# Kernel tuning notes

Measured on AMD Instinct MI355X. Metric: run time of the kernel, lower is better.

Reference implementation:

```python
import jax, jax.numpy as jnp
import numpy as np

N_NODES = 100_000
N_EDGES = 1_600_000
N_GRAPHS = 512
NF = 64        # n_node_feats
H1 = 128       # hidden width
H2 = 64        # dim_node_emb
DIM_OUT = 1
STEPS = 4      # set2set processing steps


def _lin(x, W, b):
    # torch Linear convention: y = x @ W.T + b, W: [out, in]
    return x @ W.T + b


def _gelu(x):
    return jax.nn.gelu(x, approximate=False)  # torch.nn.GELU default (erf)


def _lstm_cell(x, h, c, Wih, Whh, bih, bhh):
    g = x @ Wih.T + bih + h @ Whh.T + bhh
    i, f, gg, o = jnp.split(g, 4, axis=-1)  # torch gate order: i, f, g, o
    i, f, o = jax.nn.sigmoid(i), jax.nn.sigmoid(f), jax.nn.sigmoid(o)
    gg = jnp.tanh(gg)
    c = f * c + i * gg
    h = o * jnp.tanh(c)
    return h, c


def setup_inputs() -> dict:
    key = jax.random.key(0)
    ks = jax.random.split(key, 24)
    p = lambda k, shp: jax.random.normal(k, shp, dtype=jnp.float32) * 0.05
    inp = {
        "x": jax.random.normal(ks[0], (N_NODES, NF), dtype=jnp.float32),
        "edge_index": jax.random.randint(ks[1], (2, N_EDGES), 0, N_NODES, dtype=jnp.int32),
        "batch": jnp.sort(jax.random.randint(ks[2], (N_NODES,), 0, N_GRAPHS, dtype=jnp.int32)),
        "nfc_W": p(ks[3], (H1, NF)), "nfc_b": p(ks[4], (H1,)),
        "gc1_W": p(ks[5], (H1, H1)), "gc1_b": p(ks[6], (H1,)),
        "gc2_W": p(ks[7], (H2, H1)), "gc2_b": p(ks[8], (H2,)),
        "lstm0_Wih": p(ks[9], (4 * H2, 2 * H2)), "lstm0_Whh": p(ks[10], (4 * H2, H2)),
        "lstm0_bih": p(ks[11], (4 * H2,)), "lstm0_bhh": p(ks[12], (4 * H2,)),
        "lstm1_Wih": p(ks[13], (4 * H2, H2)), "lstm1_Whh": p(ks[14], (4 * H2, H2)),
        "lstm1_bih": p(ks[15], (4 * H2,)), "lstm1_bhh": p(ks[16], (4 * H2,)),
        "fc1_W": p(ks[17], (32, 2 * H2)), "fc1_b": p(ks[18], (32,)),
        "fc2_W": p(ks[19], (DIM_OUT, 32)), "fc2_b": p(ks[20], (DIM_OUT,)),
    }
    return inp


def _forward(x, edge_index, batch, nfc_W, nfc_b, gc1_W, gc1_b, gc2_W, gc2_b,
             lstm0_Wih, lstm0_Whh, lstm0_bih, lstm0_bhh,
             lstm1_Wih, lstm1_Whh, lstm1_bih, lstm1_bhh,
             fc1_W, fc1_b, fc2_W, fc2_b):
    src, dst = edge_index[0], edge_index[1]

    def gin_conv(h, W, b):
        # PyG GINConv, eps=0: lin((1+eps)*x + sum_{j in N(i)} x_j)
        agg = jax.ops.segment_sum(h[src], dst, num_segments=N_NODES)
        return _lin(h + agg, W, b)

    h = _gelu(_lin(x, nfc_W, nfc_b))
    h = _gelu(gin_conv(h, gc1_W, gc1_b))
    h = _gelu(gin_conv(h, gc2_W, gc2_b))
    # F.normalize(p=2, dim=1)
    h = h / jnp.maximum(jnp.linalg.norm(h, axis=1, keepdims=True), 1e-12)

    # Set2Set: 2-layer LSTM, 4 processing steps, scatter-softmax attention
    B = N_GRAPHS
    h0 = jnp.zeros((B, H2), jnp.float32); c0 = jnp.zeros((B, H2), jnp.float32)
    h1 = jnp.zeros((B, H2), jnp.float32); c1 = jnp.zeros((B, H2), jnp.float32)
    q_star = jnp.zeros((B, 2 * H2), jnp.float32)
    for _ in range(STEPS):
        h0, c0 = _lstm_cell(q_star, h0, c0, lstm0_Wih, lstm0_Whh, lstm0_bih, lstm0_bhh)
        h1, c1 = _lstm_cell(h0, h1, c1, lstm1_Wih, lstm1_Whh, lstm1_bih, lstm1_bhh)
        q = h1  # [B, H2]
        e = jnp.sum(h * q[batch], axis=-1, keepdims=True)  # [N, 1]
        m = jax.ops.segment_max(e, batch, num_segments=B)
        ex = jnp.exp(e - m[batch])
        s = jax.ops.segment_sum(ex, batch, num_segments=B)
        a = ex / (s[batch] + 1e-16)
        r = jax.ops.segment_sum(a * h, batch, num_segments=B)  # [B, H2]
        q_star = jnp.concatenate([q, r], axis=-1)

    z = _gelu(_lin(q_star, fc1_W, fc1_b))
    z = _lin(z, fc2_W, fc2_b)
    return z, h


def reference(x, edge_index, batch, nfc_W, nfc_b, gc1_W, gc1_b, gc2_W, gc2_b,
              lstm0_Wih, lstm0_Whh, lstm0_bih, lstm0_bhh,
              lstm1_Wih, lstm1_Whh, lstm1_bih, lstm1_bhh,
              fc1_W, fc1_b, fc2_W, fc2_b):
    return _forward(x, edge_index, batch, nfc_W, nfc_b, gc1_W, gc1_b, gc2_W, gc2_b,
                    lstm0_Wih, lstm0_Whh, lstm0_bih, lstm0_bhh,
                    lstm1_Wih, lstm1_Whh, lstm1_bih, lstm1_bhh,
                    fc1_W, fc1_b, fc2_W, fc2_b)
```

## Files before the change

kernel.cpp:

```cpp
#include <hip/hip_runtime.h>
#include <hip/hip_bf16.h>
#include <hip/hip_fp16.h>
#include <math.h>

constexpr int N  = 100000;
constexpr int E  = 1600000;
constexpr int NG = 512;
constexpr int NF = 64;
constexpr int H1 = 128;
constexpr int H2 = 64;

constexpr int BW   = 128;
constexpr int NB   = (N + BW - 1) / BW;
constexpr int CAP  = 2600;
constexpr int CHUNK = 4096;

constexpr int MAXN = 416;
constexpr int RST  = 68;

typedef __attribute__((ext_vector_type(8))) short short8;
typedef __attribute__((ext_vector_type(4))) float f32x4;

__device__ __forceinline__ float gelu_f(float x) {
    return 0.5f * x * (1.0f + erff(x * 0.70710678118654752f));
}
__device__ __forceinline__ float sigmoid_f(float x) {
    return 1.0f / (1.0f + expf(-x));
}
__device__ __forceinline__ float waveAllSum(float v) {
    #pragma unroll
    for (int m = 32; m; m >>= 1) v += __shfl_xor(v, m);
    return v;
}
__device__ __forceinline__ unsigned short f2bf(float x) {
    __hip_bfloat16 b = __float2bfloat16(x);
    return *reinterpret_cast<unsigned short*>(&b);
}
__device__ __forceinline__ float bf2f(unsigned short u) {
    return __uint_as_float(((unsigned int)u) << 16);
}
__device__ __forceinline__ float bf_lo(unsigned int u) { return __uint_as_float(u << 16); }
__device__ __forceinline__ float bf_hi(unsigned int u) { return __uint_as_float(u & 0xffff0000u); }

__device__ __forceinline__ void bfsplit(float v, unsigned short& hi, unsigned short& lo) {
    hi = f2bf(v);
    lo = f2bf(v - bf2f(hi));
}

__global__ __launch_bounds__(256) void setup_kernel(const int* __restrict__ batch,
                                                    const float* __restrict__ Wih0, const float* __restrict__ Whh0,
                                                    const float* __restrict__ bih0, const float* __restrict__ bhh0,
                                                    const float* __restrict__ Wih1, const float* __restrict__ Whh1,
                                                    const float* __restrict__ bih1, const float* __restrict__ bhh1,
                                                    const float* __restrict__ gc1W, const float* __restrict__ gc2W,
                                                    float* __restrict__ WT0, float* __restrict__ WT1,
                                                    float* __restrict__ b0, float* __restrict__ b1,
                                                    unsigned short* __restrict__ W1F, unsigned short* __restrict__ W2F,
                                                    int* __restrict__ bcursor, int* __restrict__ gstart) {
    int i = blockIdx.x * 256 + threadIdx.x;
    if (i < 192 * 256) {
        int k = i >> 8, j = i & 255;
        WT0[i] = (k < 128) ? Wih0[j * 128 + k] : Whh0[j * 64 + (k - 128)];
    }
    if (i < 128 * 256) {
        int k = i >> 8, j = i & 255;
        WT1[i] = (k < 64) ? Wih1[j * 64 + k] : Whh1[j * 64 + (k - 64)];
    }
    if (i < 16384) {
        int f = i >> 9, r = i & 511, l = r >> 3, j = r & 7;
        int c = f >> 3, ct = f & 7;
        int o = ct * 16 + (l & 15), k = c * 32 + (l >> 4) * 8 + j;
        unsigned short hi, lo;
        bfsplit(gc1W[o * 128 + k], hi, lo);
        W1F[f * 1024 + r] = hi;
        W1F[f * 1024 + 512 + r] = lo;
    }
    if (i < 8192) {
        int f = i >> 9, r = i & 511, l = r >> 3, j = r & 7;
        int c2 = f >> 2, ct2 = f & 3;
        int o = ct2 * 16 + (l & 15), k = c2 * 32 + (l >> 4) * 8 + j;
        unsigned short hi, lo;
        bfsplit(gc2W[o * 128 + k], hi, lo);
        W2F[f * 1024 + r] = hi;
        W2F[f * 1024 + 512 + r] = lo;
    }
    if (i < 256) { b0[i] = bih0[i] + bhh0[i]; b1[i] = bih1[i] + bhh1[i]; }
    if (i < NB) bcursor[i] = i * CAP;
    if (i <= NG) {
        if (i == NG) gstart[NG] = N;
        else {
            int lo = 0, hi = N;
            while (lo < hi) {
                int mid = (lo + hi) >> 1;
                if (batch[mid] < i) lo = mid + 1; else hi = mid;
            }
            gstart[i] = lo;
        }
    }
}

__global__ __launch_bounds__(256) void bin_scatter_kernel(const int* __restrict__ ei,
                                                          int* __restrict__ bcursor,
                                                          int* __restrict__ pairs) {
    __shared__ int hist[NB];
    __shared__ int start_s[NB];
    __shared__ int lcur[NB];
    int tid = threadIdx.x;
    int e0 = blockIdx.x * CHUNK;
    for (int b = tid; b < NB; b += 256) hist[b] = 0;
    __syncthreads();
    #pragma unroll 4
    for (int k = 0; k < CHUNK / 256; ++k) {
        int e = e0 + k * 256 + tid;
        if (e < E) atomicAdd(&hist[ei[E + e] >> 7], 1);
    }
    __syncthreads();
    for (int b = tid; b < NB; b += 256) {
        if (hist[b]) start_s[b] = atomicAdd(&bcursor[b], hist[b]);
        lcur[b] = 0;
    }
    __syncthreads();
    #pragma unroll 4
    for (int k = 0; k < CHUNK / 256; ++k) {
        int e = e0 + k * 256 + tid;
        if (e < E) {
            int d = ei[E + e];
            int s = ei[e];
            int b = d >> 7;
            int pos = start_s[b] + atomicAdd(&lcur[b], 1);
            if (pos < (b + 1) * CAP) pairs[pos] = (s << 7) | (d & 127);
        }
    }
}

__global__ __launch_bounds__(256) void csr_bucket_kernel(const int* __restrict__ pairs,
                                                         const int* __restrict__ bcursor,
                                                         int* __restrict__ srcs,
                                                         int2* __restrict__ nrange) {
    __shared__ int cnt_l[BW];
    __shared__ int cur_l[BW];
    __shared__ int wt[2];
    int b = blockIdx.x;
    int tid = threadIdx.x;
    int base = b * CAP;
    int cnt = bcursor[b] - base;
    if (cnt > CAP) cnt = CAP;
    if (tid < BW) cnt_l[tid] = 0;
    __syncthreads();
    for (int i = tid; i < cnt; i += 256) {
        atomicAdd(&cnt_l[pairs[base + i] & 127], 1);
    }
    __syncthreads();
    if (tid < BW) {
        int v = cnt_l[tid];
        int lane = tid & 63, w = tid >> 6;
        int incl = v;
        #pragma unroll
        for (int off = 1; off < 64; off <<= 1) {
            int t = __shfl_up(incl, off);
            if (lane >= off) incl += t;
        }
        if (lane == 63) wt[w] = incl;
        __syncthreads();
        int excl = (w ? wt[0] : 0) + incl - v;
        int node = b * BW + tid;
        if (node < N) nrange[node] = make_int2(base + excl, base + excl + v);
        cur_l[tid] = excl;
    } else {
        __syncthreads();
    }
    __syncthreads();
    for (int i = tid; i < cnt; i += 256) {
        int p = pairs[base + i];
        int pos = atomicAdd(&cur_l[p & 127], 1);
        srcs[base + pos] = p >> 7;
    }
}

template <int ID, int OD>
__global__ __launch_bounds__(256) void lin_mfma_kernel(const float* __restrict__ in,
                                                       const float* __restrict__ W,
                                                       const float* __restrict__ bias,
                                                       unsigned short* __restrict__ out_bf, int nrows) {
    constexpr int KC = 32;
    constexpr int NCH = ID / KC;
    constexpr int AST = 40;
    constexpr int NCT = OD / 16;
    constexpr int LDSU = 2 * 128 * AST + 2 * OD * AST;
    __shared__ __align__(16) unsigned short lds[LDSU];
    unsigned short* Ahi = lds;
    unsigned short* Alo = lds + 128 * AST;
    unsigned short* Whi = lds + 2 * 128 * AST;
    unsigned short* Wlo = lds + 2 * 128 * AST + OD * AST;

    int tid = threadIdx.x;
    int w = tid >> 6, lane = tid & 63;
    int m15 = lane & 15, quad = lane >> 4;
    int nb = blockIdx.x * 128;

    f32x4 acc[2][NCT];
    #pragma unroll
    for (int rt = 0; rt < 2; ++rt)
        #pragma unroll
        for (int ct = 0; ct < NCT; ++ct) acc[rt][ct] = (f32x4)0.f;

    for (int c = 0; c < NCH; ++c) {
        int kb = c * KC;
        #pragma unroll
        for (int it = 0; it < 4; ++it) {
            int f4 = it * 256 + tid;
            int row = f4 >> 3, kq = (f4 & 7) * 4;
            float4 v = make_float4(0.f, 0.f, 0.f, 0.f);
            if (nb + row < nrows) v = *(const float4*)&in[(size_t)(nb + row) * ID + kb + kq];
            unsigned short h0, h1, h2, h3, l0, l1, l2, l3;
            bfsplit(v.x, h0, l0); bfsplit(v.y, h1, l1);
            bfsplit(v.z, h2, l2); bfsplit(v.w, h3, l3);
            uint2 uh, ul;
            uh.x = (unsigned int)h0 | ((unsigned int)h1 << 16);
            uh.y = (unsigned int)h2 | ((unsigned int)h3 << 16);
            ul.x = (unsigned int)l0 | ((unsigned int)l1 << 16);
            ul.y = (unsigned int)l2 | ((unsigned int)l3 << 16);
            *(uint2*)&Ahi[row * AST + kq] = uh;
            *(uint2*)&Alo[row * AST + kq] = ul;
        }
        #pragma unroll
        for (int it = 0; it < OD / 32; ++it) {
            int f4 = it * 256 + tid;
            int o = f4 >> 3, kq = (f4 & 7) * 4;
            float4 v = *(const float4*)&W[(size_t)o * ID + kb + kq];
            unsigned short h0, h1, h2, h3, l0, l1, l2, l3;
            bfsplit(v.x, h0, l0); bfsplit(v.y, h1, l1);
            bfsplit(v.z, h2, l2); bfsplit(v.w, h3, l3);
            uint2 uh, ul;
            uh.x = (unsigned int)h0 | ((unsigned int)h1 << 16);
            uh.y = (unsigned int)h2 | ((unsigned int)h3 << 16);
            ul.x = (unsigned int)l0 | ((unsigned int)l1 << 16);
            ul.y = (unsigned int)l2 | ((unsigned int)l3 << 16);
            *(uint2*)&Whi[o * AST + kq] = uh;
            *(uint2*)&Wlo[o * AST + kq] = ul;
        }
        __syncthreads();

        short8 ah0 = *(const short8*)&Ahi[(w * 32 + m15) * AST + quad * 8];
        short8 ah1 = *(const short8*)&Ahi[(w * 32 + 16 + m15) * AST + quad * 8];
        short8 al0 = *(const short8*)&Alo[(w * 32 + m15) * AST + quad * 8];
        short8 al1 = *(const short8*)&Alo[(w * 32 + 16 + m15) * AST + quad * 8];
        #pragma unroll
        for (int ct = 0; ct < NCT; ++ct) {
            short8 bh = *(const short8*)&Whi[(ct * 16 + m15) * AST + quad * 8];
            short8 bl = *(const short8*)&Wlo[(ct * 16 + m15) * AST + quad * 8];
            acc[0][ct] = __builtin_amdgcn_mfma_f32_16x16x32_bf16(ah0, bh, acc[0][ct], 0, 0, 0);
            acc[0][ct] = __builtin_amdgcn_mfma_f32_16x16x32_bf16(ah0, bl, acc[0][ct], 0, 0, 0);
            acc[0][ct] = __builtin_amdgcn_mfma_f32_16x16x32_bf16(al0, bh, acc[0][ct], 0, 0, 0);
            acc[1][ct] = __builtin_amdgcn_mfma_f32_16x16x32_bf16(ah1, bh, acc[1][ct], 0, 0, 0);
            acc[1][ct] = __builtin_amdgcn_mfma_f32_16x16x32_bf16(ah1, bl, acc[1][ct], 0, 0, 0);
            acc[1][ct] = __builtin_amdgcn_mfma_f32_16x16x32_bf16(al1, bh, acc[1][ct], 0, 0, 0);
        }
        __syncthreads();
    }

    float bcol[NCT];
    #pragma unroll
    for (int ct = 0; ct < NCT; ++ct) bcol[ct] = bias[ct * 16 + m15];

    constexpr int EPS = OD + 8;
    unsigned short* ep = lds;
    #pragma unroll
    for (int rt = 0; rt < 2; ++rt)
        #pragma unroll
        for (int ct = 0; ct < NCT; ++ct)
            #pragma unroll
            for (int r = 0; r < 4; ++r) {
                int rl = w * 32 + rt * 16 + quad * 4 + r;
                float v = gelu_f(acc[rt][ct][r] + bcol[ct]);
                ep[rl * EPS + ct * 16 + m15] = f2bf(v);
            }
    __syncthreads();
    constexpr int U4 = 128 * OD / 8;
    for (int i = tid; i < U4; i += 256) {
        int row = i / (OD / 8);
        int off = (i % (OD / 8)) * 8;
        int grow = nb + row;
        if (grow < nrows) {
            uint4 v = *(const uint4*)&ep[row * EPS + off];
            *(uint4*)(out_bf + (size_t)grow * OD + off) = v;
        }
    }
}

__global__ __launch_bounds__(256) void agg_kernel(const uint2* __restrict__ hb2,
                                                  const int2* __restrict__ nrange,
                                                  const int* __restrict__ srcs,
                                                  uint4* __restrict__ utab) {
    int wave = threadIdx.x >> 6, lane = threadIdx.x & 63;
    int half = lane >> 5, hl = lane & 31;
    int n = blockIdx.x * 4 + wave;
    if (n >= N) return;
    int2 rng = nrange[n];
    int s0 = rng.x, deg = rng.y - rng.x;
    int m1 = deg < 64 ? deg : 64;
    int pre = (lane < m1) ? srcs[s0 + lane] : 0;
    float a0 = 0.f, a1 = 0.f, a2 = 0.f, a3 = 0.f;
    int t = 0;
    for (; t + 8 <= m1; t += 8) {
        int i0 = __shfl(pre, t + half);
        int i1 = __shfl(pre, t + 2 + half);
        int i2 = __shfl(pre, t + 4 + half);
        int i3 = __shfl(pre, t + 6 + half);
        uint2 u0 = hb2[(size_t)i0 * 32 + hl];
        uint2 u1 = hb2[(size_t)i1 * 32 + hl];
        uint2 u2 = hb2[(size_t)i2 * 32 + hl];
        uint2 u3 = hb2[(size_t)i3 * 32 + hl];
        a0 += bf_lo(u0.x); a1 += bf_hi(u0.x); a2 += bf_lo(u0.y); a3 += bf_hi(u0.y);
        a0 += bf_lo(u1.x); a1 += bf_hi(u1.x); a2 += bf_lo(u1.y); a3 += bf_hi(u1.y);
        a0 += bf_lo(u2.x); a1 += bf_hi(u2.x); a2 += bf_lo(u2.y); a3 += bf_hi(u2.y);
        a0 += bf_lo(u3.x); a1 += bf_hi(u3.x); a2 += bf_lo(u3.y); a3 += bf_hi(u3.y);
    }
    for (; t < m1; t += 2) {
        int idx = t + half;
        int idc = idx < m1 ? idx : 0;
        int s = __shfl(pre, idc);
        if (idx < m1) {
            uint2 u = hb2[(size_t)s * 32 + hl];
            a0 += bf_lo(u.x); a1 += bf_hi(u.x); a2 += bf_lo(u.y); a3 += bf_hi(u.y);
        }
    }
    for (int j = 64 + half; j < deg; j += 2) {
        int s = srcs[s0 + j];
        uint2 u = hb2[(size_t)s * 32 + hl];
        a0 += bf_lo(u.x); a1 += bf_hi(u.x); a2 += bf_lo(u.y); a3 += bf_hi(u.y);
    }
    a0 += __shfl_down(a0, 32);
    a1 += __shfl_down(a1, 32);
    a2 += __shfl_down(a2, 32);
    a3 += __shfl_down(a3, 32);
    if (half == 0) {
        uint2 u = hb2[(size_t)n * 32 + hl];
        a0 += bf_lo(u.x); a1 += bf_hi(u.x); a2 += bf_lo(u.y); a3 += bf_hi(u.y);
        unsigned short h0, h1, h2, h3, l0, l1, l2, l3;
        bfsplit(a0, h0, l0); bfsplit(a1, h1, l1);
        bfsplit(a2, h2, l2); bfsplit(a3, h3, l3);
        uint4 o;
        o.x = (unsigned int)h0 | ((unsigned int)h1 << 16);
        o.y = (unsigned int)h2 | ((unsigned int)h3 << 16);
        o.z = (unsigned int)l0 | ((unsigned int)l1 << 16);
        o.w = (unsigned int)l2 | ((unsigned int)l3 << 16);
        utab[(size_t)n * 32 + hl] = o;
    }
}

__global__ __launch_bounds__(256, 3) void lin2_fused_kernel(const uint4* __restrict__ in4,
                                                            const uint4* __restrict__ W1F,
                                                            const float* __restrict__ b1,
                                                            const uint4* __restrict__ W2F,
                                                            unsigned short* __restrict__ y2,
                                                            int nrows) {
    constexpr int AST2 = 40;
    __shared__ __align__(16) unsigned short lds[4 * 2560];
    union U8 { uint4 u; short8 s; };
    int tid = threadIdx.x, w = tid >> 6, lane = tid & 63;
    int m15 = lane & 15, quad = lane >> 4;
    unsigned short* myL = lds + w * 2560;
    int rowbase = blockIdx.x * 128 + w * 32;
    int r0 = rowbase + m15;      if (r0 >= nrows) r0 = nrows - 1;
    int r1 = rowbase + 16 + m15; if (r1 >= nrows) r1 = nrows - 1;
    const uint4* a0p = in4 + (size_t)r0 * 32 + quad * 2;
    const uint4* a1p = in4 + (size_t)r1 * 32 + quad * 2;

    float bc[8];
    #pragma unroll
    for (int ct = 0; ct < 8; ++ct) bc[ct] = b1[ct * 16 + m15];

    f32x4 acc[2][8];
    #pragma unroll
    for (int rt = 0; rt < 2; ++rt)
        #pragma unroll
        for (int ct = 0; ct < 8; ++ct) acc[rt][ct] = (f32x4)0.f;

    #pragma unroll
    for (int c = 0; c < 4; ++c) {
        uint4 u00 = a0p[c * 8], u01 = a0p[c * 8 + 1];
        uint4 u10 = a1p[c * 8], u11 = a1p[c * 8 + 1];
        U8 t;
        t.u = make_uint4(u00.x, u00.y, u01.x, u01.y); short8 ah0 = t.s;
        t.u = make_uint4(u00.z, u00.w, u01.z, u01.w); short8 al0 = t.s;
        t.u = make_uint4(u10.x, u10.y, u11.x, u11.y); short8 ah1 = t.s;
        t.u = make_uint4(u10.z, u10.w, u11.z, u11.w); short8 al1 = t.s;
        #pragma unroll
        for (int ct = 0; ct < 8; ++ct) {
            U8 th, tl;
            th.u = W1F[(c * 8 + ct) * 128 + lane];
            tl.u = W1F[(c * 8 + ct) * 128 + 64 + lane];
            short8 bh = th.s, bl = tl.s;
            acc[0][ct] = __builtin_amdgcn_mfma_f32_16x16x32_bf16(ah0, bh, acc[0][ct], 0, 0, 0);
            acc[0][ct] = __builtin_amdgcn_mfma_f32_16x16x32_bf16(ah0, bl, acc[0][ct], 0, 0, 0);
            acc[0][ct] = __builtin_amdgcn_mfma_f32_16x16x32_bf16(al0, bh, acc[0][ct], 0, 0, 0);
            acc[1][ct] = __builtin_amdgcn_mfma_f32_16x16x32_bf16(ah1, bh, acc[1][ct], 0, 0, 0);
            acc[1][ct] = __builtin_amdgcn_mfma_f32_16x16x32_bf16(ah1, bl, acc[1][ct], 0, 0, 0);
            acc[1][ct] = __builtin_amdgcn_mfma_f32_16x16x32_bf16(al1, bh, acc[1][ct], 0, 0, 0);
        }
    }

    #pragma unroll
    for (int ct = 0; ct < 8; ++ct)
        #pragma unroll
        for (int rt = 0; rt < 2; ++rt)
            #pragma unroll
            for (int r = 0; r < 4; ++r)
                acc[rt][ct][r] = gelu_f(acc[rt][ct][r] + bc[ct]);

    unsigned short* Ahi2 = myL;
    unsigned short* Alo2 = myL + 32 * AST2;
    f32x4 acc2[2][4];
    #pragma unroll
    for (int rt = 0; rt < 2; ++rt)
        #pragma unroll
        for (int ct = 0; ct < 4; ++ct) acc2[rt][ct] = (f32x4)0.f;

    #pragma unroll
    for (int c2 = 0; c2 < 4; ++c2) {
        #pragma unroll
        for (int rt = 0; rt < 2; ++rt)
            #pragma unroll
            for (int cc = 0; cc < 2; ++cc) {
                int ct = c2 * 2 + cc;
                #pragma unroll
                for (int r = 0; r < 4; ++r) {
                    int node = rt * 16 + quad * 4 + r;
                    unsigned short hi, lo;
                    bfsplit(acc[rt][ct][r], hi, lo);
                    Ahi2[node * AST2 + cc * 16 + m15] = hi;
                    Alo2[node * AST2 + cc * 16 + m15] = lo;
                }
            }
        asm volatile("s_waitcnt lgkmcnt(0)" ::: "memory");
        short8 ah0 = *(const short8*)&Ahi2[m15 * AST2 + quad * 8];
        short8 ah1 = *(const short8*)&Ahi2[(16 + m15) * AST2 + quad * 8];
        short8 al0 = *(const short8*)&Alo2[m15 * AST2 + quad * 8];
        short8 al1 = *(const short8*)&Alo2[(16 + m15) * AST2 + quad * 8];
        #pragma unroll
        for (int ct2 = 0; ct2 < 4; ++ct2) {
            U8 th, tl;
            th.u = W2F[(c2 * 4 + ct2) * 128 + lane];
            tl.u = W2F[(c2 * 4 + ct2) * 128 + 64 + lane];
            short8 bh = th.s, bl = tl.s;
            acc2[0][ct2] = __builtin_amdgcn_mfma_f32_16x16x32_bf16(ah0, bh, acc2[0][ct2], 0, 0, 0);
            acc2[0][ct2] = __builtin_amdgcn_mfma_f32_16x16x32_bf16(ah0, bl, acc2[0][ct2], 0, 0, 0);
            acc2[0][ct2] = __builtin_amdgcn_mfma_f32_16x16x32_bf16(al0, bh, acc2[0][ct2], 0, 0, 0);
            acc2[1][ct2] = __builtin_amdgcn_mfma_f32_16x16x32_bf16(ah1, bh, acc2[1][ct2], 0, 0, 0);
            acc2[1][ct2] = __builtin_amdgcn_mfma_f32_16x16x32_bf16(ah1, bl, acc2[1][ct2], 0, 0, 0);
            acc2[1][ct2] = __builtin_amdgcn_mfma_f32_16x16x32_bf16(al1, bh, acc2[1][ct2], 0, 0, 0);
        }
    }

    unsigned short* ep = myL;
    #pragma unroll
    for (int rt = 0; rt < 2; ++rt)
        #pragma unroll
        for (int ct2 = 0; ct2 < 4; ++ct2)
            #pragma unroll
            for (int r = 0; r < 4; ++r) {
                int node = rt * 16 + quad * 4 + r;
                __half hv = __float2half(acc2[rt][ct2][r]);
                ep[node * 72 + ct2 * 16 + m15] = *reinterpret_cast<unsigned short*>(&hv);
            }
    asm volatile("s_waitcnt lgkmcnt(0)" ::: "memory");
    #pragma unroll
    for (int it = 0; it < 4; ++it) {
        int idx = it * 64 + lane;
        int rowl = idx >> 3, off = (idx & 7) * 8;
        int grow = rowbase + rowl;
        if (grow < nrows)
            *(uint4*)(y2 + (size_t)grow * 64 + off) = *(const uint4*)&ep[rowl * 72 + off];
    }
}

__global__ __launch_bounds__(256) void agg2_norm_kernel(const uint2* __restrict__ y2,
                                                        const int2* __restrict__ nrange,
                                                        const int* __restrict__ srcs,
                                                        const float* __restrict__ b2,
                                                        float* __restrict__ hn) {
    int wave = threadIdx.x >> 6, lane = threadIdx.x & 63;
    int qw = lane >> 4, ql = lane & 15;
    int n = blockIdx.x * 4 + wave;
    if (n >= N) return;
    int2 rng = nrange[n];
    int s0 = rng.x, deg = rng.y - rng.x;
    int m1 = deg < 64 ? deg : 64;
    int pre = (lane < m1) ? srcs[s0 + lane] : 0;
    float a0 = 0.f, a1 = 0.f, a2 = 0.f, a3 = 0.f;
    auto addu = [&](uint2 u) {
        float2 f01 = __half22float2(*reinterpret_cast<__half2*>(&u.x));
        float2 f23 = __half22float2(*reinterpret_cast<__half2*>(&u.y));
        a0 += f01.x; a1 += f01.y; a2 += f23.x; a3 += f23.y;
    };
    int t = 0;
    for (; t + 8 <= m1; t += 8) {
        int i0 = __shfl(pre, t + qw);
        int i1 = __shfl(pre, t + 4 + qw);
        uint2 u0 = y2[(size_t)i0 * 16 + ql];
        uint2 u1 = y2[(size_t)i1 * 16 + ql];
        addu(u0); addu(u1);
    }
    for (; t < m1; t += 4) {
        int idx = t + qw;
        int s = __shfl(pre, idx < m1 ? idx : 0);
        if (idx < m1) addu(y2[(size_t)s * 16 + ql]);
    }
    for (int j = 64 + qw; j < deg; j += 4) addu(y2[(size_t)srcs[s0 + j] * 16 + ql]);
    a0 += __shfl_down(a0, 32); a1 += __shfl_down(a1, 32);
    a2 += __shfl_down(a2, 32); a3 += __shfl_down(a3, 32);
    a0 += __shfl_down(a0, 16); a1 += __shfl_down(a1, 16);
    a2 += __shfl_down(a2, 16); a3 += __shfl_down(a3, 16);
    if (qw == 0) {
        addu(y2[(size_t)n * 16 + ql]);
        float4 bv = *(const float4*)&b2[ql * 4];
        float v0 = gelu_f(a0 + bv.x), v1 = gelu_f(a1 + bv.y);
        float v2 = gelu_f(a2 + bv.z), v3 = gelu_f(a3 + bv.w);
        float ss = v0 * v0 + v1 * v1 + v2 * v2 + v3 * v3;
        #pragma unroll
        for (int mm = 1; mm < 16; mm <<= 1) ss += __shfl_xor(ss, mm);
        float d = fmaxf(sqrtf(ss), 1e-12f);
        *(float4*)&hn[(size_t)n * 64 + ql * 4] = make_float4(v0 / d, v1 / d, v2 / d, v3 / d);
    }
}

__global__ __launch_bounds__(256) void set2set_kernel(const float* __restrict__ hn,
                                                      const int* __restrict__ gstart,
                                                      const float* __restrict__ WT0, const float* __restrict__ b0,
                                                      const float* __restrict__ WT1, const float* __restrict__ b1,
                                                      float* __restrict__ qstar_out) {
    __shared__ __align__(16) unsigned short hL[MAXN * RST];
    __shared__ float av[MAXN];
    __shared__ __align__(16) float xc0[192];
    __shared__ __align__(16) float xc1[128];
    __shared__ __align__(16) float gates[256];
    __shared__ float c0v[H2], c1v[H2];
    __shared__ float red[4];
    __shared__ float rp[4][H2];
    __shared__ float sp[4];

    int g = blockIdx.x;
    int tid = threadIdx.x, w = tid >> 6, lane = tid & 63;
    int s0 = gstart[g], s1 = gstart[g + 1];
    int cnt = s1 - s0;
    int cL = cnt < MAXN ? cnt : MAXN;
    const float* hq = xc1 + 64;

    for (int idx = tid; idx < cL * 16; idx += 256) {
        int n = idx >> 4, p4 = idx & 15;
        float4 v = *(const float4*)&hn[(size_t)(s0 + n) * 64 + p4 * 4];
        uint2 u;
        u.x = (unsigned int)f2bf(v.x) | ((unsigned int)f2bf(v.y) << 16);
        u.y = (unsigned int)f2bf(v.z) | ((unsigned int)f2bf(v.w) << 16);
        *(uint2*)&hL[n * RST + p4 * 4] = u;
    }
    if (tid < 192) xc0[tid] = 0.f;
    if (tid < 128) xc1[tid] = 0.f;
    if (tid < H2) { c0v[tid] = 0.f; c1v[tid] = 0.f; }
    float b0v = b0[tid], b1v = b1[tid];
    __syncthreads();

    for (int step = 0; step < 4; ++step) {
        {
            float a0 = 0.f, a1 = 0.f, a2 = 0.f, a3 = 0.f;
            #pragma unroll 8
            for (int k = 0; k < 192; k += 4) {
                a0 += xc0[k]     * WT0[(k)     * 256 + tid];
                a1 += xc0[k + 1] * WT0[(k + 1) * 256 + tid];
                a2 += xc0[k + 2] * WT0[(k + 2) * 256 + tid];
                a3 += xc0[k + 3] * WT0[(k + 3) * 256 + tid];
            }
            gates[tid] = (a0 + a1) + (a2 + a3) + b0v;
        }
        __syncthreads();
        if (tid < H2) {
            float ii = sigmoid_f(gates[tid]), ff = sigmoid_f(gates[H2 + tid]);
            float gg = tanhf(gates[2 * H2 + tid]), oo = sigmoid_f(gates[3 * H2 + tid]);
            float c = ff * c0v[tid] + ii * gg;
            float h = oo * tanhf(c);
            c0v[tid] = c; xc0[128 + tid] = h; xc1[tid] = h;
        }
        __syncthreads();
        {
            float a0 = 0.f, a1 = 0.f, a2 = 0.f, a3 = 0.f;
            #pragma unroll 8
            for (int k = 0; k < 128; k += 4) {
                a0 += xc1[k]     * WT1[(k)     * 256 + tid];
                a1 += xc1[k + 1] * WT1[(k + 1) * 256 + tid];
                a2 += xc1[k + 2] * WT1[(k + 2) * 256 + tid];
                a3 += xc1[k + 3] * WT1[(k + 3) * 256 + tid];
            }
            gates[tid] = (a0 + a1) + (a2 + a3) + b1v;
        }
        __syncthreads();
        if (tid < H2) {
            float ii = sigmoid_f(gates[tid]), ff = sigmoid_f(gates[H2 + tid]);
            float gg = tanhf(gates[2 * H2 + tid]), oo = sigmoid_f(gates[3 * H2 + tid]);
            float c = ff * c1v[tid] + ii * gg;
            float h = oo * tanhf(c);
            c1v[tid] = c; xc1[64 + tid] = h;
        }
        __syncthreads();

        float lm = -INFINITY;
        for (int i = tid; i < cnt; i += 256) {
            float e = 0.f;
            if (i < MAXN) {
                const uint2* row = (const uint2*)&hL[i * RST];
                #pragma unroll
                for (int p4 = 0; p4 < 16; ++p4) {
                    uint2 u = row[p4];
                    e += bf_lo(u.x) * hq[p4 * 4 + 0];
                    e += bf_hi(u.x) * hq[p4 * 4 + 1];
                    e += bf_lo(u.y) * hq[p4 * 4 + 2];
                    e += bf_hi(u.y) * hq[p4 * 4 + 3];
                }
                av[i] = e;
            } else {
                for (int f = 0; f < 64; ++f) e += hn[(size_t)(s0 + i) * 64 + f] * hq[f];
            }
            lm = fmaxf(lm, e);
        }
        #pragma unroll
        for (int mm = 32; mm; mm >>= 1) lm = fmaxf(lm, __shfl_xor(lm, mm));
        if (lane == 0) red[w] = lm;
        __syncthreads();
        float m = fmaxf(fmaxf(red[0], red[1]), fmaxf(red[2], red[3]));

        float ps = 0.f;
        for (int i = tid; i < cnt; i += 256) {
            float e;
            if (i < MAXN) e = av[i];
            else {
                e = 0.f;
                for (int f = 0; f < 64; ++f) e += hn[(size_t)(s0 + i) * 64 + f] * hq[f];
            }
            float p = expf(e - m);
            ps += p;
            if (i < MAXN) av[i] = p;
        }
        ps = waveAllSum(ps);
        if (lane == 0) sp[w] = ps;
        __syncthreads();
        float s = sp[0] + sp[1] + sp[2] + sp[3];

        float racc = 0.f;
        for (int i = w; i < cL; i += 4) {
            unsigned short hv = hL[i * RST + lane];
            racc += av[i] * bf2f(hv);
        }
        float qf = hq[lane];
        for (int n = MAXN + w; n < cnt; n += 4) {
            float v = hn[(size_t)(s0 + n) * 64 + lane];
            float e = waveAllSum(v * qf);
            float p = expf(e - m);
            racc += p * v;
        }
        rp[w][lane] = racc;
        __syncthreads();
        if (tid < H2) {
            float r = 0.f;
            if (cnt > 0) {
                r = (rp[0][tid] + rp[1][tid] + rp[2][tid] + rp[3][tid]) / (s + 1e-16f);
            }
            xc0[tid] = xc1[64 + tid];
            xc0[H2 + tid] = r;
        }
        __syncthreads();
    }
    if (tid < 2 * H2) qstar_out[g * 2 * H2 + tid] = xc0[tid];
}

__global__ __launch_bounds__(256) void fcout_kernel(const float* __restrict__ q_star,
                                                    const float* __restrict__ W1, const float* __restrict__ b1,
                                                    const float* __restrict__ W2, const float* __restrict__ b2,
                                                    float* __restrict__ z) {
    __shared__ float W1l[32 * 128];
    __shared__ float b1l[32], W2l[32];
    int tid = threadIdx.x;
    for (int i = tid; i < 32 * 128; i += 256) W1l[i] = W1[i];
    if (tid < 32) { b1l[tid] = b1[tid]; W2l[tid] = W2[tid]; }
    __syncthreads();
    int g = blockIdx.x * 256 + tid;
    float acc[32];
    #pragma unroll
    for (int j = 0; j < 32; ++j) acc[j] = b1l[j];
    for (int k = 0; k < 128; ++k) {
        float qv = q_star[g * 128 + k];
        #pragma unroll
        for (int j = 0; j < 32; ++j) acc[j] += qv * W1l[j * 128 + k];
    }
    float zv = b2[0];
    #pragma unroll
    for (int j = 0; j < 32; ++j) zv += gelu_f(acc[j]) * W2l[j];
    z[g] = zv;
}

extern "C" void kernel_launch(void* const* d_in, const int* in_sizes, int n_in,
                              void* d_out, int out_size, void* d_ws, size_t ws_size,
                              hipStream_t stream) {
    const float* x       = (const float*)d_in[0];
    const int*   ei      = (const int*)d_in[1];
    const int*   batch   = (const int*)d_in[2];
    const float* nfc_W   = (const float*)d_in[3];
    const float* nfc_b   = (const float*)d_in[4];
    const float* gc1_W   = (const float*)d_in[5];
    const float* gc1_b   = (const float*)d_in[6];
    const float* gc2_W   = (const float*)d_in[7];
    const float* gc2_b   = (const float*)d_in[8];
    const float* l0_Wih  = (const float*)d_in[9];
    const float* l0_Whh  = (const float*)d_in[10];
    const float* l0_bih  = (const float*)d_in[11];
    const float* l0_bhh  = (const float*)d_in[12];
    const float* l1_Wih  = (const float*)d_in[13];
    const float* l1_Whh  = (const float*)d_in[14];
    const float* l1_bih  = (const float*)d_in[15];
    const float* l1_bhh  = (const float*)d_in[16];
    const float* fc1_W   = (const float*)d_in[17];
    const float* fc1_b   = (const float*)d_in[18];
    const float* fc2_W   = (const float*)d_in[19];
    const float* fc2_b   = (const float*)d_in[20];

    float* out = (float*)d_out;
    float* hn_out = out + NG;

    char* p = (char*)d_ws;
    auto take = [&](size_t bytes) {
        char* r = p;
        p += (bytes + 255) & ~size_t(255);
        return r;
    };
    float*          sbuf  = (float*)take((size_t)N * H1 * 4);
    unsigned short* hbbuf = (unsigned short*)take((size_t)N * H1 * 2);
    int*   srcs   = (int*)take((size_t)NB * CAP * 4);
    int2*  nrange = (int2*)take((size_t)N * 8);
    int*   bcursor= (int*)take((size_t)NB * 4);
    int*   gstart = (int*)take((size_t)(NG + 1) * 4);
    float* qstar  = (float*)take((size_t)NG * 2 * H2 * 4);
    float* WT0    = (float*)take((size_t)192 * 256 * 4);
    float* WT1    = (float*)take((size_t)128 * 256 * 4);
    float* b0     = (float*)take((size_t)256 * 4);
    float* b1     = (float*)take((size_t)256 * 4);
    unsigned short* W1F = (unsigned short*)take((size_t)32 * 1024 * 2);
    unsigned short* W2F = (unsigned short*)take((size_t)16 * 1024 * 2);

    int* pairs = (int*)sbuf;

    setup_kernel<<<192, 256, 0, stream>>>(batch, l0_Wih, l0_Whh, l0_bih, l0_bhh,
                                          l1_Wih, l1_Whh, l1_bih, l1_bhh,
                                          gc1_W, gc2_W,
                                          WT0, WT1, b0, b1, W1F, W2F, bcursor, gstart);

    bin_scatter_kernel<<<(E + CHUNK - 1) / CHUNK, 256, 0, stream>>>(ei, bcursor, pairs);
    csr_bucket_kernel<<<NB, 256, 0, stream>>>(pairs, bcursor, srcs, nrange);

    int mfmaGrid = (N + 127) / 128;
    lin_mfma_kernel<NF, H1><<<mfmaGrid, 256, 0, stream>>>(x, nfc_W, nfc_b, hbbuf, N);
    agg_kernel<<<(N + 3) / 4, 256, 0, stream>>>((const uint2*)hbbuf, nrange, srcs, (uint4*)sbuf);
    lin2_fused_kernel<<<mfmaGrid, 256, 0, stream>>>((const uint4*)sbuf, (const uint4*)W1F, gc1_b,
                                                    (const uint4*)W2F, hbbuf, N);
    agg2_norm_kernel<<<(N + 3) / 4, 256, 0, stream>>>((const uint2*)hbbuf, nrange, srcs,
                                                      gc2_b, hn_out);

    set2set_kernel<<<NG, 256, 0, stream>>>(hn_out, gstart, WT0, b0, WT1, b1, qstar);

    fcout_kernel<<<2, 256, 0, stream>>>(qstar, fc1_W, fc1_b, fc2_W, fc2_b, out);
}
```

Measured before the change: 470.2 us.

## Fuse first GIN aggregation into MLP kernel and pre-pack input linear weights

The neighbor-sum aggregation for the first GIN layer is fused into the gc1/gc2 MFMA kernel. Each wave gathers 32 nodes' neighborhoods into a swizzled LDS slab and prefetches the next node's source list, which removes the full-width split-bf16 intermediate round trip through global memory. The input linear layer now reads pre-split bf16 weight fragments prepared in setup and loads x directly into registers instead of staging through LDS with block barriers. The cost is that each wave aggregates its 32 nodes serially with lower occupancy (launch bound 2), so gather latency may be less well hidden than with the previous one-node-per-wave kernel. A separate y2 buffer is also added so the second layer no longer overwrites hbbuf.

```diff
diff --git a/kernel.cpp b/kernel.cpp
--- a/kernel.cpp
+++ b/kernel.cpp
@@ -47,15 +47,29 @@
     lo = f2bf(v - bf2f(hi));
 }
 
+__device__ __forceinline__ void pack8(float4 a, float4 b, short8& h8, short8& l8) {
+    unsigned short h0,h1,h2,h3,h4,h5,h6,h7,l0,l1,l2,l3,l4,l5,l6,l7;
+    bfsplit(a.x,h0,l0); bfsplit(a.y,h1,l1); bfsplit(a.z,h2,l2); bfsplit(a.w,h3,l3);
+    bfsplit(b.x,h4,l4); bfsplit(b.y,h5,l5); bfsplit(b.z,h6,l6); bfsplit(b.w,h7,l7);
+    union { uint4 u; short8 s; } th, tl;
+    th.u = make_uint4((unsigned)h0|((unsigned)h1<<16),(unsigned)h2|((unsigned)h3<<16),
+                      (unsigned)h4|((unsigned)h5<<16),(unsigned)h6|((unsigned)h7<<16));
+    tl.u = make_uint4((unsigned)l0|((unsigned)l1<<16),(unsigned)l2|((unsigned)l3<<16),
+                      (unsigned)l4|((unsigned)l5<<16),(unsigned)l6|((unsigned)l7<<16));
+    h8 = th.s; l8 = tl.s;
+}
+
 __global__ __launch_bounds__(256) void setup_kernel(const int* __restrict__ batch,
                                                     const float* __restrict__ Wih0, const float* __restrict__ Whh0,
                                                     const float* __restrict__ bih0, const float* __restrict__ bhh0,
                                                     const float* __restrict__ Wih1, const float* __restrict__ Whh1,
                                                     const float* __restrict__ bih1, const float* __restrict__ bhh1,
                                                     const float* __restrict__ gc1W, const float* __restrict__ gc2W,
+                                                    const float* __restrict__ nfcW,
                                                     float* __restrict__ WT0, float* __restrict__ WT1,
                                                     float* __restrict__ b0, float* __restrict__ b1,
                                                     unsigned short* __restrict__ W1F, unsigned short* __restrict__ W2F,
+                                                    unsigned short* __restrict__ W0F,
                                                     int* __restrict__ bcursor, int* __restrict__ gstart) {
     int i = blockIdx.x * 256 + threadIdx.x;
     if (i < 192 * 256) {
@@ -83,6 +97,15 @@
         bfsplit(gc2W[o * 128 + k], hi, lo);
         W2F[f * 1024 + r] = hi;
         W2F[f * 1024 + 512 + r] = lo;
+    }
+    if (i < 8192) {
+        int f = i >> 9, r = i & 511, l = r >> 3, j = r & 7;
+        int c = f >> 3, ct = f & 7;
+        int o = ct * 16 + (l & 15), k = c * 32 + (l >> 4) * 8 + j;
+        unsigned short hi, lo;
+        bfsplit(nfcW[o * 64 + k], hi, lo);
+        W0F[f * 1024 + r] = hi;
+        W0F[f * 1024 + 512 + r] = lo;
     }
     if (i < 256) { b0[i] = bih0[i] + bhh0[i]; b1[i] = bih1[i] + bhh1[i]; }
     if (i < NB) bcursor[i] = i * CAP;
@@ -177,78 +200,40 @@
     }
 }
 
-template <int ID, int OD>
-__global__ __launch_bounds__(256) void lin_mfma_kernel(const float* __restrict__ in,
-                                                       const float* __restrict__ W,
-                                                       const float* __restrict__ bias,
-                                                       unsigned short* __restrict__ out_bf, int nrows) {
-    constexpr int KC = 32;
-    constexpr int NCH = ID / KC;
-    constexpr int AST = 40;
-    constexpr int NCT = OD / 16;
-    constexpr int LDSU = 2 * 128 * AST + 2 * OD * AST;
-    __shared__ __align__(16) unsigned short lds[LDSU];
-    unsigned short* Ahi = lds;
-    unsigned short* Alo = lds + 128 * AST;
-    unsigned short* Whi = lds + 2 * 128 * AST;
-    unsigned short* Wlo = lds + 2 * 128 * AST + OD * AST;
-
-    int tid = threadIdx.x;
-    int w = tid >> 6, lane = tid & 63;
+__global__ __launch_bounds__(256, 3) void lin1_kernel(const float* __restrict__ x,
+                                                      const uint4* __restrict__ W0F,
+                                                      const float* __restrict__ bias,
+                                                      unsigned short* __restrict__ out_bf, int nrows) {
+    constexpr int EPS = 136;
+    __shared__ __align__(16) unsigned short eps[4][32 * EPS];
+    union U8 { uint4 u; short8 s; };
+    int tid = threadIdx.x, w = tid >> 6, lane = tid & 63;
     int m15 = lane & 15, quad = lane >> 4;
-    int nb = blockIdx.x * 128;
-
-    f32x4 acc[2][NCT];
+    int rowbase = blockIdx.x * 128 + w * 32;
+    int r0 = rowbase + m15;      if (r0 >= nrows) r0 = nrows - 1;
+    int r1 = rowbase + 16 + m15; if (r1 >= nrows) r1 = nrows - 1;
+
+    f32x4 acc[2][8];
     #pragma unroll
     for (int rt = 0; rt < 2; ++rt)
         #pragma unroll
-        for (int ct = 0; ct < NCT; ++ct) acc[rt][ct] = (f32x4)0.f;
-
-    for (int c = 0; c < NCH; ++c) {
-        int kb = c * KC;
-        #pragma unroll
-        for (int it = 0; it < 4; ++it) {
-            int f4 = it * 256 + tid;
-            int row = f4 >> 3, kq = (f4 & 7) * 4;
-            float4 v = make_float4(0.f, 0.f, 0.f, 0.f);
-            if (nb + row < nrows) v = *(const float4*)&in[(size_t)(nb + row) * ID + kb + kq];
-            unsigned short h0, h1, h2, h3, l0, l1, l2, l3;
-            bfsplit(v.x, h0, l0); bfsplit(v.y, h1, l1);
-            bfsplit(v.z, h2, l2); bfsplit(v.w, h3, l3);
-            uint2 uh, ul;
-            uh.x = (unsigned int)h0 | ((unsigned int)h1 << 16);
-            uh.y = (unsigned int)h2 | ((unsigned int)h3 << 16);
-            ul.x = (unsigned int)l0 | ((unsigned int)l1 << 16);
-            ul.y = (unsigned int)l2 | ((unsigned int)l3 << 16);
-            *(uint2*)&Ahi[row * AST + kq] = uh;
-            *(uint2*)&Alo[row * AST + kq] = ul;
-        }
-        #pragma unroll
-        for (int it = 0; it < OD / 32; ++it) {
-            int f4 = it * 256 + tid;
-            int o = f4 >> 3, kq = (f4 & 7) * 4;
-            float4 v = *(const float4*)&W[(size_t)o * ID + kb + kq];
-            unsigned short h0, h1, h2, h3, l0, l1, l2, l3;
-            bfsplit(v.x, h0, l0); bfsplit(v.y, h1, l1);
-            bfsplit(v.z, h2, l2); bfsplit(v.w, h3, l3);
-            uint2 uh, ul;
-            uh.x = (unsigned int)h0 | ((unsigned int)h1 << 16);
-            uh.y = (unsigned int)h2 | ((unsigned int)h3 << 16);
-            ul.x = (unsigned int)l0 | ((unsigned int)l1 << 16);
-            ul.y = (unsigned int)l2 | ((unsigned int)l3 << 16);
-            *(uint2*)&Whi[o * AST + kq] = uh;
-            *(uint2*)&Wlo[o * AST + kq] = ul;
-        }
-        __syncthreads();
-
-        short8 ah0 = *(const short8*)&Ahi[(w * 32 + m15) * AST + quad * 8];
-        short8 ah1 = *(const short8*)&Ahi[(w * 32 + 16 + m15) * AST + quad * 8];
-        short8 al0 = *(const short8*)&Alo[(w * 32 + m15) * AST + quad * 8];
-        short8 al1 = *(const short8*)&Alo[(w * 32 + 16 + m15) * AST + quad * 8];
-        #pragma unroll
-        for (int ct = 0; ct < NCT; ++ct) {
-            short8 bh = *(const short8*)&Whi[(ct * 16 + m15) * AST + quad * 8];
-            short8 bl = *(const short8*)&Wlo[(ct * 16 + m15) * AST + quad * 8];
+        for (int ct = 0; ct < 8; ++ct) acc[rt][ct] = (f32x4)0.f;
+
+    #pragma unroll
+    for (int c = 0; c < 2; ++c) {
+        float4 p00 = *(const float4*)&x[(size_t)r0 * 64 + c * 32 + quad * 8];
+        float4 p01 = *(const float4*)&x[(size_t)r0 * 64 + c * 32 + quad * 8 + 4];
+        float4 p10 = *(const float4*)&x[(size_t)r1 * 64 + c * 32 + quad * 8];
+        float4 p11 = *(const float4*)&x[(size_t)r1 * 64 + c * 32 + quad * 8 + 4];
+        short8 ah0, al0, ah1, al1;
+        pack8(p00, p01, ah0, al0);
+        pack8(p10, p11, ah1, al1);
+        #pragma unroll
+        for (int ct = 0; ct < 8; ++ct) {
+            U8 th, tl;
+            th.u = W0F[(c * 8 + ct) * 128 + lane];
+            tl.u = W0F[(c * 8 + ct) * 128 + 64 + lane];
+            short8 bh = th.s, bl = tl.s;
             acc[0][ct] = __builtin_amdgcn_mfma_f32_16x16x32_bf16(ah0, bh, acc[0][ct], 0, 0, 0);
             acc[0][ct] = __builtin_amdgcn_mfma_f32_16x16x32_bf16(ah0, bl, acc[0][ct], 0, 0, 0);
             acc[0][ct] = __builtin_amdgcn_mfma_f32_16x16x32_bf16(al0, bh, acc[0][ct], 0, 0, 0);
@@ -256,116 +241,121 @@
             acc[1][ct] = __builtin_amdgcn_mfma_f32_16x16x32_bf16(ah1, bl, acc[1][ct], 0, 0, 0);
             acc[1][ct] = __builtin_amdgcn_mfma_f32_16x16x32_bf16(al1, bh, acc[1][ct], 0, 0, 0);
         }
-        __syncthreads();
-    }
-
-    float bcol[NCT];
-    #pragma unroll
-    for (int ct = 0; ct < NCT; ++ct) bcol[ct] = bias[ct * 16 + m15];
-
-    constexpr int EPS = OD + 8;
-    unsigned short* ep = lds;
-    #pragma unroll
-    for (int rt = 0; rt < 2; ++rt)
-        #pragma unroll
-        for (int ct = 0; ct < NCT; ++ct)
+    }
+
+    unsigned short* ep = eps[w];
+    #pragma unroll
+    for (int ct = 0; ct < 8; ++ct) {
+        float bc = bias[ct * 16 + m15];
+        #pragma unroll
+        for (int rt = 0; rt < 2; ++rt)
             #pragma unroll
             for (int r = 0; r < 4; ++r) {
-                int rl = w * 32 + rt * 16 + quad * 4 + r;
-                float v = gelu_f(acc[rt][ct][r] + bcol[ct]);
-                ep[rl * EPS + ct * 16 + m15] = f2bf(v);
-            }
-    __syncthreads();
-    constexpr int U4 = 128 * OD / 8;
-    for (int i = tid; i < U4; i += 256) {
-        int row = i / (OD / 8);
-        int off = (i % (OD / 8)) * 8;
-        int grow = nb + row;
-        if (grow < nrows) {
-            uint4 v = *(const uint4*)&ep[row * EPS + off];
-            *(uint4*)(out_bf + (size_t)grow * OD + off) = v;
-        }
-    }
-}
-
-__global__ __launch_bounds__(256) void agg_kernel(const uint2* __restrict__ hb2,
-                                                  const int2* __restrict__ nrange,
-                                                  const int* __restrict__ srcs,
-                                                  uint4* __restrict__ utab) {
-    int wave = threadIdx.x >> 6, lane = threadIdx.x & 63;
-    int half = lane >> 5, hl = lane & 31;
-    int n = blockIdx.x * 4 + wave;
-    if (n >= N) return;
-    int2 rng = nrange[n];
-    int s0 = rng.x, deg = rng.y - rng.x;
-    int m1 = deg < 64 ? deg : 64;
-    int pre = (lane < m1) ? srcs[s0 + lane] : 0;
-    float a0 = 0.f, a1 = 0.f, a2 = 0.f, a3 = 0.f;
-    int t = 0;
-    for (; t + 8 <= m1; t += 8) {
-        int i0 = __shfl(pre, t + half);
-        int i1 = __shfl(pre, t + 2 + half);
-        int i2 = __shfl(pre, t + 4 + half);
-        int i3 = __shfl(pre, t + 6 + half);
-        uint2 u0 = hb2[(size_t)i0 * 32 + hl];
-        uint2 u1 = hb2[(size_t)i1 * 32 + hl];
-        uint2 u2 = hb2[(size_t)i2 * 32 + hl];
-        uint2 u3 = hb2[(size_t)i3 * 32 + hl];
-        a0 += bf_lo(u0.x); a1 += bf_hi(u0.x); a2 += bf_lo(u0.y); a3 += bf_hi(u0.y);
-        a0 += bf_lo(u1.x); a1 += bf_hi(u1.x); a2 += bf_lo(u1.y); a3 += bf_hi(u1.y);
-        a0 += bf_lo(u2.x); a1 += bf_hi(u2.x); a2 += bf_lo(u2.y); a3 += bf_hi(u2.y);
-        a0 += bf_lo(u3.x); a1 += bf_hi(u3.x); a2 += bf_lo(u3.y); a3 += bf_hi(u3.y);
-    }
-    for (; t < m1; t += 2) {
-        int idx = t + half;
-        int idc = idx < m1 ? idx : 0;
-        int s = __shfl(pre, idc);
-        if (idx < m1) {
-            uint2 u = hb2[(size_t)s * 32 + hl];
-            a0 += bf_lo(u.x); a1 += bf_hi(u.x); a2 += bf_lo(u.y); a3 += bf_hi(u.y);
-        }
-    }
-    for (int j = 64 + half; j < deg; j += 2) {
-        int s = srcs[s0 + j];
-        uint2 u = hb2[(size_t)s * 32 + hl];
-        a0 += bf_lo(u.x); a1 += bf_hi(u.x); a2 += bf_lo(u.y); a3 += bf_hi(u.y);
-    }
-    a0 += __shfl_down(a0, 32);
-    a1 += __shfl_down(a1, 32);
-    a2 += __shfl_down(a2, 32);
-    a3 += __shfl_down(a3, 32);
-    if (half == 0) {
-        uint2 u = hb2[(size_t)n * 32 + hl];
-        a0 += bf_lo(u.x); a1 += bf_hi(u.x); a2 += bf_lo(u.y); a3 += bf_hi(u.y);
-        unsigned short h0, h1, h2, h3, l0, l1, l2, l3;
-        bfsplit(a0, h0, l0); bfsplit(a1, h1, l1);
-        bfsplit(a2, h2, l2); bfsplit(a3, h3, l3);
-        uint4 o;
-        o.x = (unsigned int)h0 | ((unsigned int)h1 << 16);
-        o.y = (unsigned int)h2 | ((unsigned int)h3 << 16);
-        o.z = (unsigned int)l0 | ((unsigned int)l1 << 16);
-        o.w = (unsigned int)l2 | ((unsigned int)l3 << 16);
-        utab[(size_t)n * 32 + hl] = o;
-    }
-}
-
-__global__ __launch_bounds__(256, 3) void lin2_fused_kernel(const uint4* __restrict__ in4,
-                                                            const uint4* __restrict__ W1F,
-                                                            const float* __restrict__ b1,
-                                                            const uint4* __restrict__ W2F,
-                                                            unsigned short* __restrict__ y2,
-                                                            int nrows) {
-    constexpr int AST2 = 40;
-    __shared__ __align__(16) unsigned short lds[4 * 2560];
+                int node = rt * 16 + quad * 4 + r;
+                ep[node * EPS + ct * 16 + m15] = f2bf(gelu_f(acc[rt][ct][r] + bc));
+            }
+    }
+    asm volatile("s_waitcnt lgkmcnt(0)" ::: "memory");
+    #pragma unroll
+    for (int it = 0; it < 8; ++it) {
+        int idx = it * 64 + lane;
+        int rowl = idx >> 4, off = (idx & 15) * 8;
+        int grow = rowbase + rowl;
+        if (grow < nrows)
+            *(uint4*)(out_bf + (size_t)grow * 128 + off) = *(const uint4*)&ep[rowl * EPS + off];
+    }
+}
+
+__global__ __launch_bounds__(256, 2) void aggin2_kernel(const uint2* __restrict__ hb2,
+                                                        const int2* __restrict__ nrange,
+                                                        const int* __restrict__ srcs,
+                                                        const uint4* __restrict__ W1F,
+                                                        const float* __restrict__ b1,
+                                                        const uint4* __restrict__ W2F,
+                                                        unsigned short* __restrict__ y2,
+                                                        int nrows) {
+    __shared__ uint4 slab[4][32][32];
     union U8 { uint4 u; short8 s; };
     int tid = threadIdx.x, w = tid >> 6, lane = tid & 63;
     int m15 = lane & 15, quad = lane >> 4;
-    unsigned short* myL = lds + w * 2560;
+    int half = lane >> 5, hl = lane & 31;
     int rowbase = blockIdx.x * 128 + w * 32;
-    int r0 = rowbase + m15;      if (r0 >= nrows) r0 = nrows - 1;
-    int r1 = rowbase + 16 + m15; if (r1 >= nrows) r1 = nrows - 1;
-    const uint4* a0p = in4 + (size_t)r0 * 32 + quad * 2;
-    const uint4* a1p = in4 + (size_t)r1 * 32 + quad * 2;
+
+    int ra = 0, rb = 0;
+    if (lane < 32) {
+        int n = rowbase + lane;
+        if (n < nrows) { int2 t = nrange[n]; ra = t.x; rb = t.y; }
+    }
+    int s0c = __shfl(ra, 0), e0c = __shfl(rb, 0);
+    int degc = e0c - s0c;
+    int m1c = degc < 64 ? degc : 64;
+    int prec = (lane < m1c) ? srcs[s0c + lane] : 0;
+
+    for (int i = 0; i < 32; ++i) {
+        int s0n = 0, degn = 0, m1n = 0, pren = 0;
+        if (i < 31) {
+            s0n = __shfl(ra, i + 1);
+            int e = __shfl(rb, i + 1);
+            degn = e - s0n;
+            m1n = degn < 64 ? degn : 64;
+            pren = (lane < m1n) ? srcs[s0n + lane] : 0;
+        }
+        int n = rowbase + i;
+        float a0 = 0.f, a1 = 0.f, a2 = 0.f, a3 = 0.f;
+        if (n < nrows) {
+            int t = 0;
+            for (; t + 8 <= m1c; t += 8) {
+                int i0 = __shfl(prec, t + half);
+                int i1 = __shfl(prec, t + 2 + half);
+                int i2 = __shfl(prec, t + 4 + half);
+                int i3 = __shfl(prec, t + 6 + half);
+                uint2 u0 = hb2[(size_t)i0 * 32 + hl];
+                uint2 u1 = hb2[(size_t)i1 * 32 + hl];
+                uint2 u2 = hb2[(size_t)i2 * 32 + hl];
+                uint2 u3 = hb2[(size_t)i3 * 32 + hl];
+                a0 += bf_lo(u0.x); a1 += bf_hi(u0.x); a2 += bf_lo(u0.y); a3 += bf_hi(u0.y);
+                a0 += bf_lo(u1.x); a1 += bf_hi(u1.x); a2 += bf_lo(u1.y); a3 += bf_hi(u1.y);
+                a0 += bf_lo(u2.x); a1 += bf_hi(u2.x); a2 += bf_lo(u2.y); a3 += bf_hi(u2.y);
+                a0 += bf_lo(u3.x); a1 += bf_hi(u3.x); a2 += bf_lo(u3.y); a3 += bf_hi(u3.y);
+            }
+            for (; t < m1c; t += 2) {
+                int idx = t + half;
+                int idc = idx < m1c ? idx : 0;
+                int s = __shfl(prec, idc);
+                if (idx < m1c) {
+                    uint2 u = hb2[(size_t)s * 32 + hl];
+                    a0 += bf_lo(u.x); a1 += bf_hi(u.x); a2 += bf_lo(u.y); a3 += bf_hi(u.y);
+                }
+            }
+            for (int j = 64 + half; j < degc; j += 2) {
+                int s = srcs[s0c + j];
+                uint2 u = hb2[(size_t)s * 32 + hl];
+                a0 += bf_lo(u.x); a1 += bf_hi(u.x); a2 += bf_lo(u.y); a3 += bf_hi(u.y);
+            }
+            a0 += __shfl_down(a0, 32);
+            a1 += __shfl_down(a1, 32);
+            a2 += __shfl_down(a2, 32);
+            a3 += __shfl_down(a3, 32);
+        }
+        if (half == 0) {
+            uint4 o = make_uint4(0u, 0u, 0u, 0u);
+            if (n < nrows) {
+                uint2 u = hb2[(size_t)n * 32 + hl];
+                a0 += bf_lo(u.x); a1 += bf_hi(u.x); a2 += bf_lo(u.y); a3 += bf_hi(u.y);
+                unsigned short h0, h1, h2, h3, l0, l1, l2, l3;
+                bfsplit(a0, h0, l0); bfsplit(a1, h1, l1);
+                bfsplit(a2, h2, l2); bfsplit(a3, h3, l3);
+                o.x = (unsigned)h0 | ((unsigned)h1 << 16);
+                o.y = (unsigned)h2 | ((unsigned)h3 << 16);
+                o.z = (unsigned)l0 | ((unsigned)l1 << 16);
+                o.w = (unsigned)l2 | ((unsigned)l3 << 16);
+            }
+            slab[w][i][hl ^ (i & 7)] = o;
+        }
+        prec = pren; s0c = s0n; degc = degn; m1c = m1n;
+    }
+    asm volatile("s_waitcnt lgkmcnt(0)" ::: "memory");
+    __builtin_amdgcn_sched_barrier(0);
 
     float bc[8];
     #pragma unroll
@@ -377,10 +367,14 @@
         #pragma unroll
         for (int ct = 0; ct < 8; ++ct) acc[rt][ct] = (f32x4)0.f;
 
+    int swz = m15 & 7;
     #pragma unroll
     for (int c = 0; c < 4; ++c) {
-        uint4 u00 = a0p[c * 8], u01 = a0p[c * 8 + 1];
-        uint4 u10 = a1p[c * 8], u11 = a1p[c * 8 + 1];
+        int g0 = c * 8 + quad * 2;
+        uint4 u00 = slab[w][m15][(g0) ^ swz];
+        uint4 u01 = slab[w][m15][(g0 + 1) ^ swz];
+        uint4 u10 = slab[w][16 + m15][(g0) ^ swz];
+        uint4 u11 = slab[w][16 + m15][(g0 + 1) ^ swz];
         U8 t;
         t.u = make_uint4(u00.x, u00.y, u01.x, u01.y); short8 ah0 = t.s;
         t.u = make_uint4(u00.z, u00.w, u01.z, u01.w); short8 al0 = t.s;
@@ -409,6 +403,8 @@
             for (int r = 0; r < 4; ++r)
                 acc[rt][ct][r] = gelu_f(acc[rt][ct][r] + bc[ct]);
 
+    constexpr int AST2 = 40;
+    unsigned short* myL = (unsigned short*)&slab[w][0][0];
     unsigned short* Ahi2 = myL;
     unsigned short* Alo2 = myL + 32 * AST2;
     f32x4 acc2[2][4];
@@ -731,8 +727,9 @@
         p += (bytes + 255) & ~size_t(255);
         return r;
     };
-    float*          sbuf  = (float*)take((size_t)N * H1 * 4);
+    int*            pairs = (int*)take((size_t)NB * CAP * 4);
     unsigned short* hbbuf = (unsigned short*)take((size_t)N * H1 * 2);
+    unsigned short* y2buf = (unsigned short*)take((size_t)N * H2 * 2);
     int*   srcs   = (int*)take((size_t)NB * CAP * 4);
     int2*  nrange = (int2*)take((size_t)N * 8);
     int*   bcursor= (int*)take((size_t)NB * 4);
@@ -744,23 +741,22 @@
     float* b1     = (float*)take((size_t)256 * 4);
     unsigned short* W1F = (unsigned short*)take((size_t)32 * 1024 * 2);
     unsigned short* W2F = (unsigned short*)take((size_t)16 * 1024 * 2);
-
-    int* pairs = (int*)sbuf;
+    unsigned short* W0F = (unsigned short*)take((size_t)16 * 1024 * 2);
 
     setup_kernel<<<192, 256, 0, stream>>>(batch, l0_Wih, l0_Whh, l0_bih, l0_bhh,
                                           l1_Wih, l1_Whh, l1_bih, l1_bhh,
-                                          gc1_W, gc2_W,
-                                          WT0, WT1, b0, b1, W1F, W2F, bcursor, gstart);
+                                          gc1_W, gc2_W, nfc_W,
+                                          WT0, WT1, b0, b1, W1F, W2F, W0F, bcursor, gstart);
 
     bin_scatter_kernel<<<(E + CHUNK - 1) / CHUNK, 256, 0, stream>>>(ei, bcursor, pairs);
     csr_bucket_kernel<<<NB, 256, 0, stream>>>(pairs, bcursor, srcs, nrange);
 
     int mfmaGrid = (N + 127) / 128;
-    lin_mfma_kernel<NF, H1><<<mfmaGrid, 256, 0, stream>>>(x, nfc_W, nfc_b, hbbuf, N);
-    agg_kernel<<<(N + 3) / 4, 256, 0, stream>>>((const uint2*)hbbuf, nrange, srcs, (uint4*)sbuf);
-    lin2_fused_kernel<<<mfmaGrid, 256, 0, stream>>>((const uint4*)sbuf, (const uint4*)W1F, gc1_b,
-                                                    (const uint4*)W2F, hbbuf, N);
-    agg2_norm_kernel<<<(N + 3) / 4, 256, 0, stream>>>((const uint2*)hbbuf, nrange, srcs,
+    lin1_kernel<<<mfmaGrid, 256, 0, stream>>>(x, (const uint4*)W0F, nfc_b, hbbuf, N);
+    aggin2_kernel<<<mfmaGrid, 256, 0, stream>>>((const uint2*)hbbuf, nrange, srcs,
+                                                (const uint4*)W1F, gc1_b, (const uint4*)W2F,
+                                                y2buf, N);
+    agg2_norm_kernel<<<(N + 3) / 4, 256, 0, stream>>>((const uint2*)y2buf, nrange, srcs,
                                                       gc2_b, hn_out);
 
     set2set_kernel<<<NG, 256, 0, stream>>>(hn_out, gstart, WT0, b0, WT1, b1, qstar);
```

Measured after the change: 494.5 us. 1.05x slower.
